# Optimization experiments

Hardware: AMD Instinct MI355X
Metric: run time of the kernel (lower is better)

## Reference

```python
import jax, jax.numpy as jnp
import numpy as np

B, S, D = 8, 4096, 256


def setup_inputs() -> dict:
    key = jax.random.key(0)
    kq, kk, kv, kb = jax.random.split(key, 4)
    q = jax.random.normal(kq, (B, S, D), dtype=jnp.float32)
    k = jax.random.normal(kk, (B, S, D), dtype=jnp.float32)
    v = jax.random.normal(kv, (B, S, D), dtype=jnp.float32)
    beta = jax.random.uniform(kb, (B, S), dtype=jnp.float32)
    return {"q": q, "k": k, "v": v, "beta": beta}


def reference(q, k, v, beta):
    # Delta-rule linear attention recurrence:
    #   h_t = beta_t * h_{t-1} + k_t^T v_t   (h: [B, D, D])
    #   o_t = q_t @ h_t                      (o: [B, D])
    dtype = q.dtype
    b, s, d = q.shape
    h0 = jnp.zeros((b, d, d), dtype=dtype)

    def step(h, inp):
        q_t, k_t, v_t, b_t = inp  # q_t/k_t/v_t: [B, D], b_t: [B]
        h = h * b_t[:, None, None] + jnp.einsum('bi,bj->bij', k_t, v_t)
        o_t = jnp.einsum('bi,bij->bj', q_t, h)
        return h, o_t

    xs = (q.transpose(1, 0, 2), k.transpose(1, 0, 2),
          v.transpose(1, 0, 2), beta.T)  # time-major
    _, out = jax.lax.scan(step, h0, xs)  # out: [S, B, D]
    return out.transpose(1, 0, 2)  # [B, S, D]
```

## Files before the change

### kernel.cpp

```cpp
#include <hip/hip_runtime.h>
#include <hip/hip_bf16.h>
#include <math.h>


#define B_ 8
#define S_ 4096
#define D_ 256
#define L_ 128
#define C_ (S_ / L_)
#define BC_ (B_ * C_)
#define STK 66

typedef __attribute__((ext_vector_type(8))) short s8v;
typedef __attribute__((ext_vector_type(4))) float f4v;
typedef unsigned short u16;
typedef unsigned int u32;

__device__ __forceinline__ u32 pk2(float lo, float hi) {
  union { __hip_bfloat162 h; u32 u; } cv;
  cv.h = __float22bfloat162_rn(make_float2(lo, hi));
  return cv.u;
}
__device__ __forceinline__ s8v pack8(const float4 a, const float4 b) {
  union { u32 u[4]; s8v v; } r;
  r.u[0] = pk2(a.x, a.y); r.u[1] = pk2(a.z, a.w);
  r.u[2] = pk2(b.x, b.y); r.u[3] = pk2(b.z, b.w);
  return r.v;
}

__global__ __launch_bounds__(512, 4) void ks_summary8(
    const float* __restrict__ kg, const float* __restrict__ vg,
    const float* __restrict__ beta, u16* __restrict__ A,
    float* __restrict__ P)
{
  __shared__ float ls[L_];
  __shared__ __align__(16) u16 U[2][256 * STK];

  const int bc = blockIdx.x;
  const int b = bc / C_, c = bc % C_;
  const int tid = threadIdx.x;
  const float* betap = beta + (size_t)b * S_ + (size_t)c * L_;
  const float* kbase = kg + ((size_t)b * S_ + (size_t)c * L_) * D_;
  const float* vbase = vg + ((size_t)b * S_ + (size_t)c * L_) * D_;

  const int hh = tid >> 8;
  const int t2 = tid & 255;
  const int iLs = t2 & 7;
  const int s0s = (t2 >> 3) * 2;
  const int sg = hh * 64 + s0s;

  float bx0 = 1.f, bx1 = 1.f;
  if (tid < 64) { bx0 = betap[tid]; bx1 = betap[64 + tid]; }

  float4 kp[16];
  {
    const float* k0 = kbase + (size_t)sg * D_;
#pragma unroll
    for (int p = 0; p < 8; ++p) {
      const int i0 = p * 32 + iLs * 4;
      kp[2 * p]     = *(const float4*)(k0 + i0);
      kp[2 * p + 1] = *(const float4*)(k0 + D_ + i0);
    }
  }

  if (tid < 64) {
    float x = log2f(fmaxf(bx0, 1e-30f));
#pragma unroll
    for (int off = 1; off < 64; off <<= 1) {
      float y = __shfl_up(x, off);
      if (tid >= off) x += y;
    }
    ls[tid] = x;
    const float tot0 = __shfl(x, 63);
    float z = log2f(fmaxf(bx1, 1e-30f));
#pragma unroll
    for (int off = 1; off < 64; off <<= 1) {
      float y = __shfl_up(z, off);
      if (tid >= off) z += y;
    }
    ls[64 + tid] = z + tot0;
  }
  __syncthreads();
  const float ltot = ls[L_ - 1];
  if (tid == 0) P[bc] = exp2f(ltot);

  {
    const float w0 = exp2f(ltot - ls[sg]);
    const float w1 = exp2f(ltot - ls[sg + 1]);
    u16* dst = U[hh];
#pragma unroll
    for (int p = 0; p < 8; ++p) {
      const int i0 = p * 32 + iLs * 4;
      const float4 a0 = kp[2 * p], a1 = kp[2 * p + 1];
      *(u32*)&dst[(i0 + 0) * STK + s0s] = pk2(a0.x * w0, a1.x * w1);
      *(u32*)&dst[(i0 + 1) * STK + s0s] = pk2(a0.y * w0, a1.y * w1);
      *(u32*)&dst[(i0 + 2) * STK + s0s] = pk2(a0.z * w0, a1.z * w1);
      *(u32*)&dst[(i0 + 3) * STK + s0s] = pk2(a0.w * w0, a1.w * w1);
    }
  }
  __syncthreads();

  const int lane = tid & 63, wave = tid >> 6;
  const int quad = lane >> 4, l15 = lane & 15;
  const int i0w = wave * 32;

  float4 vb[8];
  {
    const float* v0 = vbase + (size_t)sg * D_;
#pragma unroll
    for (int p = 0; p < 4; ++p) {
      const int i0 = p * 32 + iLs * 4;
      vb[2 * p]     = *(const float4*)(v0 + i0);
      vb[2 * p + 1] = *(const float4*)(v0 + D_ + i0);
    }
  }

  s8v af[2][4];
#pragma unroll
  for (int mt = 0; mt < 2; ++mt)
#pragma unroll
    for (int ks = 0; ks < 4; ++ks)
      af[mt][ks] = *(const s8v*)&U[ks >> 1][(i0w + mt * 16 + l15) * STK +
                                            (ks & 1) * 32 + quad * 8];
  __syncthreads();

  {
    u16* dst = U[hh];
#pragma unroll
    for (int p = 0; p < 4; ++p) {
      const int i0 = p * 32 + iLs * 4;
      const float4 a0 = vb[2 * p], a1 = vb[2 * p + 1];
      *(u32*)&dst[(i0 + 0) * STK + s0s] = pk2(a0.x, a1.x);
      *(u32*)&dst[(i0 + 1) * STK + s0s] = pk2(a0.y, a1.y);
      *(u32*)&dst[(i0 + 2) * STK + s0s] = pk2(a0.z, a1.z);
      *(u32*)&dst[(i0 + 3) * STK + s0s] = pk2(a0.w, a1.w);
    }
    const float* v0 = vbase + (size_t)sg * D_;
#pragma unroll
    for (int p = 4; p < 8; ++p) {
      const int i0 = p * 32 + iLs * 4;
      const float4 a0 = *(const float4*)(v0 + i0);
      const float4 a1 = *(const float4*)(v0 + D_ + i0);
      *(u32*)&dst[(i0 + 0) * STK + s0s] = pk2(a0.x, a1.x);
      *(u32*)&dst[(i0 + 1) * STK + s0s] = pk2(a0.y, a1.y);
      *(u32*)&dst[(i0 + 2) * STK + s0s] = pk2(a0.z, a1.z);
      *(u32*)&dst[(i0 + 3) * STK + s0s] = pk2(a0.w, a1.w);
    }
  }
  __syncthreads();

  u16* Ab = A + (size_t)bc * D_ * D_;

  for (int ng = 0; ng < 4; ++ng) {
    f4v acc[2][4];
#pragma unroll
    for (int mt = 0; mt < 2; ++mt)
#pragma unroll
      for (int nt = 0; nt < 4; ++nt) acc[mt][nt] = (f4v){0.f, 0.f, 0.f, 0.f};

#pragma unroll
    for (int ks = 0; ks < 4; ++ks) {
      const int so = (ks & 1) * 32 + quad * 8;
      s8v bv[4];
#pragma unroll
      for (int nt = 0; nt < 4; ++nt)
        bv[nt] = *(const s8v*)&U[ks >> 1][(ng * 64 + nt * 16 + l15) * STK + so];
#pragma unroll
      for (int mt = 0; mt < 2; ++mt)
#pragma unroll
        for (int nt = 0; nt < 4; ++nt)
          acc[mt][nt] = __builtin_amdgcn_mfma_f32_16x16x32_bf16(
              af[mt][ks], bv[nt], acc[mt][nt], 0, 0, 0);
    }
#pragma unroll
    for (int mt = 0; mt < 2; ++mt)
#pragma unroll
      for (int nt = 0; nt < 4; ++nt) {
        const int jl = ng * 64 + nt * 16 + l15;
        uint2 w;
        w.x = pk2(acc[mt][nt][0], acc[mt][nt][1]);
        w.y = pk2(acc[mt][nt][2], acc[mt][nt][3]);
        *(uint2*)&Ab[(size_t)jl * D_ + i0w + mt * 16 + quad * 4] = w;
      }
  }
}

__global__ __launch_bounds__(256) void ks_scan8(
    u16* __restrict__ A, const float* __restrict__ P)
{
  const int g = blockIdx.x;
  const int b = g >> 6;
  const int unit = ((g & 63) << 8) + threadIdx.x;
  u16* base = A + (size_t)b * ((size_t)C_ * D_ * D_) + (size_t)unit * 4;
  const float* Pb = P + b * C_;

  uint2 d[C_];
#pragma unroll
  for (int c = 0; c < C_; ++c)
    d[c] = *(const uint2*)(base + (size_t)c * (D_ * D_));

  float h0 = 0.f, h1 = 0.f, h2 = 0.f, h3 = 0.f;
#pragma unroll
  for (int c = 0; c < C_; ++c) {
    const float pc = Pb[c];
    const uint2 u = d[c];
    const float a0 = __uint_as_float(u.x << 16);
    const float a1 = __uint_as_float(u.x & 0xFFFF0000u);
    const float a2 = __uint_as_float(u.y << 16);
    const float a3 = __uint_as_float(u.y & 0xFFFF0000u);
    d[c].x = pk2(h0, h1);
    d[c].y = pk2(h2, h3);
    h0 = fmaf(pc, h0, a0); h1 = fmaf(pc, h1, a1);
    h2 = fmaf(pc, h2, a2); h3 = fmaf(pc, h3, a3);
  }
#pragma unroll
  for (int c = 0; c < C_; ++c)
    *(uint2*)(base + (size_t)c * (D_ * D_)) = d[c];
}

__global__ __launch_bounds__(512, 2) void ks_output8(
    const float* __restrict__ qg, const float* __restrict__ kg,
    const float* __restrict__ vg, const float* __restrict__ beta,
    const u16* __restrict__ Hg, float* __restrict__ outg)
{
  __shared__ float ls[L_];
  __shared__ float cv[L_];
  __shared__ __align__(16) u16 QB[L_ * 264];
  __shared__ __align__(16) u16 Tm[L_ * 136];
  __shared__ __align__(16) u16 VT[256 * STK];

  const int bc = blockIdx.x;
  const int b = bc / C_, c = bc % C_;
  const int tid = threadIdx.x;
  const float* betap = beta + (size_t)b * S_ + (size_t)c * L_;
  const float* qbase = qg + ((size_t)b * S_ + (size_t)c * L_) * D_;
  const float* kbase = kg + ((size_t)b * S_ + (size_t)c * L_) * D_;
  const float* vbase = vg + ((size_t)b * S_ + (size_t)c * L_) * D_;
  const u16* Hb = Hg + (size_t)bc * D_ * D_;

  float bx0 = 1.f, bx1 = 1.f;
  if (tid < 64) { bx0 = betap[tid]; bx1 = betap[64 + tid]; }

  const int qt = tid >> 2, qc = (tid & 3) * 8;
  float4 qp[16];
  {
    const float* src = qbase + (size_t)qt * D_ + qc;
#pragma unroll
    for (int p = 0; p < 8; ++p) {
      qp[2 * p]     = *(const float4*)(src + p * 32);
      qp[2 * p + 1] = *(const float4*)(src + p * 32 + 4);
    }
  }
  const int iL3 = tid & 15;
  const int s03 = ((tid >> 4) & 31) * 2;
  float4 vp0[8];
  {
    const float* a0 = vbase + (size_t)s03 * D_;
#pragma unroll
    for (int p = 0; p < 4; ++p) {
      const int i0 = p * 64 + iL3 * 4;
      vp0[2 * p]     = *(const float4*)(a0 + i0);
      vp0[2 * p + 1] = *(const float4*)(a0 + D_ + i0);
    }
  }

  if (tid < 64) {
    float x = log2f(fmaxf(bx0, 1e-30f));
#pragma unroll
    for (int off = 1; off < 64; off <<= 1) {
      float y = __shfl_up(x, off);
      if (tid >= off) x += y;
    }
    ls[tid] = x;
    const float tot0 = __shfl(x, 63);
    float z = log2f(fmaxf(bx1, 1e-30f));
#pragma unroll
    for (int off = 1; off < 64; off <<= 1) {
      float y = __shfl_up(z, off);
      if (tid >= off) z += y;
    }
    ls[64 + tid] = z + tot0;
  }

#pragma unroll
  for (int p = 0; p < 8; ++p)
    *(s8v*)&QB[qt * 264 + qc + p * 32] = pack8(qp[2 * p], qp[2 * p + 1]);
  __syncthreads();
  if (tid < L_) cv[tid] = exp2f(ls[tid]);

  const int lane = tid & 63, wave = tid >> 6;
  const int quad = lane >> 4, l15 = lane & 15;
  const int j0w = wave * 32;

  {
    const int mA = wave * 16;
    f4v accA[8];
#pragma unroll
    for (int i = 0; i < 8; ++i) accA[i] = (f4v){0.f, 0.f, 0.f, 0.f};
#pragma unroll
    for (int kd = 0; kd < 8; ++kd) {
      const int d0 = kd * 32 + quad * 8;
      const float* krow = kbase + (size_t)(mA + l15) * D_ + d0;
      const s8v afr = pack8(*(const float4*)krow, *(const float4*)(krow + 4));
#pragma unroll
      for (int nt = 0; nt < 8; ++nt) {
        const s8v bf = *(const s8v*)&QB[(nt * 16 + l15) * 264 + d0];
        accA[nt] = __builtin_amdgcn_mfma_f32_16x16x32_bf16(afr, bf, accA[nt],
                                                           0, 0, 0);
      }
    }
#pragma unroll
    for (int nt = 0; nt < 8; ++nt) {
      const int t = nt * 16 + l15;
      const float lt = ls[t];
      const int s0 = mA + quad * 4;
      float v4[4];
#pragma unroll
      for (int r = 0; r < 4; ++r) {
        const int s = s0 + r;
        v4[r] = (s <= t) ? accA[nt][r] * exp2f(lt - ls[s]) : 0.f;
      }
      uint2 w;
      w.x = pk2(v4[0], v4[1]);
      w.y = pk2(v4[2], v4[3]);
      *(uint2*)&Tm[t * 136 + s0] = w;
    }
  }

  {
#pragma unroll
    for (int p = 0; p < 4; ++p) {
      const int i0 = p * 64 + iL3 * 4;
      const float4 a0 = vp0[2 * p], a1 = vp0[2 * p + 1];
      *(u32*)&VT[(i0 + 0) * STK + s03] = pk2(a0.x, a1.x);
      *(u32*)&VT[(i0 + 1) * STK + s03] = pk2(a0.y, a1.y);
      *(u32*)&VT[(i0 + 2) * STK + s03] = pk2(a0.z, a1.z);
      *(u32*)&VT[(i0 + 3) * STK + s03] = pk2(a0.w, a1.w);
    }
  }

  s8v hc[2];
#pragma unroll
  for (int mt = 0; mt < 2; ++mt)
    hc[mt] = *(const s8v*)(Hb + (size_t)(j0w + mt * 16 + l15) * D_ + quad * 8);

  __syncthreads();

  float4 vp1[8];
  {
    const float* b0 = vbase + (size_t)(64 + s03) * D_;
#pragma unroll
    for (int p = 0; p < 4; ++p) {
      const int i0 = p * 64 + iL3 * 4;
      vp1[2 * p]     = *(const float4*)(b0 + i0);
      vp1[2 * p + 1] = *(const float4*)(b0 + D_ + i0);
    }
  }

  f4v acc[2][8];
#pragma unroll
  for (int mt = 0; mt < 2; ++mt)
#pragma unroll
    for (int nt = 0; nt < 8; ++nt) acc[mt][nt] = (f4v){0.f, 0.f, 0.f, 0.f};

#pragma unroll
  for (int ks = 0; ks < 8; ++ks) {
    const int io = ks * 32 + quad * 8;
    s8v hn[2] = {hc[0], hc[1]};
    if (ks < 7) {
#pragma unroll
      for (int mt = 0; mt < 2; ++mt)
        hn[mt] = *(const s8v*)(Hb + (size_t)(j0w + mt * 16 + l15) * D_ +
                               io + 32);
    }
    s8v bfq[8];
#pragma unroll
    for (int nt = 0; nt < 8; ++nt)
      bfq[nt] = *(const s8v*)&QB[(nt * 16 + l15) * 264 + io];
#pragma unroll
    for (int mt = 0; mt < 2; ++mt)
#pragma unroll
      for (int nt = 0; nt < 8; ++nt)
        acc[mt][nt] = __builtin_amdgcn_mfma_f32_16x16x32_bf16(
            hc[mt], bfq[nt], acc[mt][nt], 0, 0, 0);
    hc[0] = hn[0]; hc[1] = hn[1];
  }
#pragma unroll
  for (int nt = 0; nt < 8; ++nt) {
    const float ct = cv[nt * 16 + l15];
#pragma unroll
    for (int mt = 0; mt < 2; ++mt) {
      acc[mt][nt][0] *= ct; acc[mt][nt][1] *= ct;
      acc[mt][nt][2] *= ct; acc[mt][nt][3] *= ct;
    }
  }

#pragma unroll
  for (int ks = 0; ks < 2; ++ks) {
    const int so = ks * 32 + quad * 8;
    s8v afv[2], bfv[8];
#pragma unroll
    for (int mt = 0; mt < 2; ++mt)
      afv[mt] = *(const s8v*)&VT[(j0w + mt * 16 + l15) * STK + so];
#pragma unroll
    for (int nt = 0; nt < 8; ++nt)
      bfv[nt] = *(const s8v*)&Tm[(nt * 16 + l15) * 136 + so];
#pragma unroll
    for (int mt = 0; mt < 2; ++mt)
#pragma unroll
      for (int nt = 0; nt < 8; ++nt)
        acc[mt][nt] = __builtin_amdgcn_mfma_f32_16x16x32_bf16(
            afv[mt], bfv[nt], acc[mt][nt], 0, 0, 0);
  }

  __syncthreads();
  {
#pragma unroll
    for (int p = 0; p < 4; ++p) {
      const int i0 = p * 64 + iL3 * 4;
      const float4 a0 = vp1[2 * p], a1 = vp1[2 * p + 1];
      *(u32*)&VT[(i0 + 0) * STK + s03] = pk2(a0.x, a1.x);
      *(u32*)&VT[(i0 + 1) * STK + s03] = pk2(a0.y, a1.y);
      *(u32*)&VT[(i0 + 2) * STK + s03] = pk2(a0.z, a1.z);
      *(u32*)&VT[(i0 + 3) * STK + s03] = pk2(a0.w, a1.w);
    }
  }
  __syncthreads();
#pragma unroll
  for (int ks = 0; ks < 2; ++ks) {
    const int so = ks * 32 + quad * 8;
    s8v afv[2], bfv[8];
#pragma unroll
    for (int mt = 0; mt < 2; ++mt)
      afv[mt] = *(const s8v*)&VT[(j0w + mt * 16 + l15) * STK + so];
#pragma unroll
    for (int nt = 0; nt < 8; ++nt)
      bfv[nt] = *(const s8v*)&Tm[(nt * 16 + l15) * 136 + 64 + so];
#pragma unroll
    for (int mt = 0; mt < 2; ++mt)
#pragma unroll
      for (int nt = 0; nt < 8; ++nt)
        acc[mt][nt] = __builtin_amdgcn_mfma_f32_16x16x32_bf16(
            afv[mt], bfv[nt], acc[mt][nt], 0, 0, 0);
  }

  float* ob = outg + ((size_t)b * S_ + (size_t)c * L_) * D_;
#pragma unroll
  for (int mt = 0; mt < 2; ++mt)
#pragma unroll
    for (int nt = 0; nt < 8; ++nt) {
      const int t = nt * 16 + l15;
      const int j0 = j0w + mt * 16 + quad * 4;
      float4 o;
      o.x = acc[mt][nt][0]; o.y = acc[mt][nt][1];
      o.z = acc[mt][nt][2]; o.w = acc[mt][nt][3];
      *(float4*)(ob + (size_t)t * D_ + j0) = o;
    }
}

extern "C" void kernel_launch(void* const* d_in, const int* in_sizes, int n_in,
                              void* d_out, int out_size, void* d_ws,
                              size_t ws_size, hipStream_t stream) {
  const float* q = (const float*)d_in[0];
  const float* k = (const float*)d_in[1];
  const float* v = (const float*)d_in[2];
  const float* beta = (const float*)d_in[3];
  float* out = (float*)d_out;

  u16* A = (u16*)d_ws;
  float* P = (float*)((char*)d_ws + (size_t)BC_ * D_ * D_ * sizeof(u16));

  ks_summary8<<<dim3(BC_), dim3(512), 0, stream>>>(k, v, beta, A, P);
  ks_scan8<<<dim3(512), dim3(256), 0, stream>>>(A, P);
  ks_output8<<<dim3(BC_), dim3(512), 0, stream>>>(q, k, v, beta, A, out);
}
```

Before: 173.7 us.

## Alias output-kernel shared buffers and defer V transpose to raise occupancy

The output kernel now overlays the Q tile, the V-transpose tile and the intra-chunk score tile in one shared array, cutting LDS per block roughly in half. The intra-chunk scores stay packed in registers until after the H·Q product, and the V load and transpose are moved after that GEMM. The launch bound is raised to 4 blocks per CU, and the cumulative-decay exponentials are computed inside the prefix-scan wave. The grid has only 256 blocks, so the added occupancy may go unused. The tighter register budget, with a 64-register accumulator plus the held score registers, risks spilling.

```diff
diff --git a/kernel.cpp b/kernel.cpp
--- a/kernel.cpp
+++ b/kernel.cpp
@@ -28,7 +28,7 @@
   return r.v;
 }
 
-__global__ __launch_bounds__(512, 4) void ks_summary8(
+__global__ __launch_bounds__(512, 4) void ks_summary9(
     const float* __restrict__ kg, const float* __restrict__ vg,
     const float* __restrict__ beta, u16* __restrict__ A,
     float* __restrict__ P)
@@ -185,7 +185,7 @@
   }
 }
 
-__global__ __launch_bounds__(256) void ks_scan8(
+__global__ __launch_bounds__(256) void ks_scan9(
     u16* __restrict__ A, const float* __restrict__ P)
 {
   const int g = blockIdx.x;
@@ -218,16 +218,14 @@
     *(uint2*)(base + (size_t)c * (D_ * D_)) = d[c];
 }
 
-__global__ __launch_bounds__(512, 2) void ks_output8(
+__global__ __launch_bounds__(512, 4) void ks_output9(
     const float* __restrict__ qg, const float* __restrict__ kg,
     const float* __restrict__ vg, const float* __restrict__ beta,
     const u16* __restrict__ Hg, float* __restrict__ outg)
 {
   __shared__ float ls[L_];
   __shared__ float cv[L_];
-  __shared__ __align__(16) u16 QB[L_ * 264];
-  __shared__ __align__(16) u16 Tm[L_ * 136];
-  __shared__ __align__(16) u16 VT[256 * STK];
+  __shared__ __align__(16) u16 raw[34304];
 
   const int bc = blockIdx.x;
   const int b = bc / C_, c = bc % C_;
@@ -251,18 +249,6 @@
       qp[2 * p + 1] = *(const float4*)(src + p * 32 + 4);
     }
   }
-  const int iL3 = tid & 15;
-  const int s03 = ((tid >> 4) & 31) * 2;
-  float4 vp0[8];
-  {
-    const float* a0 = vbase + (size_t)s03 * D_;
-#pragma unroll
-    for (int p = 0; p < 4; ++p) {
-      const int i0 = p * 64 + iL3 * 4;
-      vp0[2 * p]     = *(const float4*)(a0 + i0);
-      vp0[2 * p + 1] = *(const float4*)(a0 + D_ + i0);
-    }
-  }
 
   if (tid < 64) {
     float x = log2f(fmaxf(bx0, 1e-30f));
@@ -272,6 +258,7 @@
       if (tid >= off) x += y;
     }
     ls[tid] = x;
+    cv[tid] = exp2f(x);
     const float tot0 = __shfl(x, 63);
     float z = log2f(fmaxf(bx1, 1e-30f));
 #pragma unroll
@@ -280,20 +267,22 @@
       if (tid >= off) z += y;
     }
     ls[64 + tid] = z + tot0;
-  }
-
+    cv[64 + tid] = exp2f(z + tot0);
+  }
+
+  u16* QB = raw;
 #pragma unroll
   for (int p = 0; p < 8; ++p)
     *(s8v*)&QB[qt * 264 + qc + p * 32] = pack8(qp[2 * p], qp[2 * p + 1]);
   __syncthreads();
-  if (tid < L_) cv[tid] = exp2f(ls[tid]);
 
   const int lane = tid & 63, wave = tid >> 6;
   const int quad = lane >> 4, l15 = lane & 15;
   const int j0w = wave * 32;
-
-  {
-    const int mA = wave * 16;
+  const int mA = wave * 16;
+
+  uint2 tpk[8];
+  {
     f4v accA[8];
 #pragma unroll
     for (int i = 0; i < 8; ++i) accA[i] = (f4v){0.f, 0.f, 0.f, 0.f};
@@ -320,22 +309,8 @@
         const int s = s0 + r;
         v4[r] = (s <= t) ? accA[nt][r] * exp2f(lt - ls[s]) : 0.f;
       }
-      uint2 w;
-      w.x = pk2(v4[0], v4[1]);
-      w.y = pk2(v4[2], v4[3]);
-      *(uint2*)&Tm[t * 136 + s0] = w;
-    }
-  }
-
-  {
-#pragma unroll
-    for (int p = 0; p < 4; ++p) {
-      const int i0 = p * 64 + iL3 * 4;
-      const float4 a0 = vp0[2 * p], a1 = vp0[2 * p + 1];
-      *(u32*)&VT[(i0 + 0) * STK + s03] = pk2(a0.x, a1.x);
-      *(u32*)&VT[(i0 + 1) * STK + s03] = pk2(a0.y, a1.y);
-      *(u32*)&VT[(i0 + 2) * STK + s03] = pk2(a0.z, a1.z);
-      *(u32*)&VT[(i0 + 3) * STK + s03] = pk2(a0.w, a1.w);
+      tpk[nt].x = pk2(v4[0], v4[1]);
+      tpk[nt].y = pk2(v4[2], v4[3]);
     }
   }
 
@@ -343,19 +318,6 @@
 #pragma unroll
   for (int mt = 0; mt < 2; ++mt)
     hc[mt] = *(const s8v*)(Hb + (size_t)(j0w + mt * 16 + l15) * D_ + quad * 8);
-
-  __syncthreads();
-
-  float4 vp1[8];
-  {
-    const float* b0 = vbase + (size_t)(64 + s03) * D_;
-#pragma unroll
-    for (int p = 0; p < 4; ++p) {
-      const int i0 = p * 64 + iL3 * 4;
-      vp1[2 * p]     = *(const float4*)(b0 + i0);
-      vp1[2 * p + 1] = *(const float4*)(b0 + D_ + i0);
-    }
-  }
 
   f4v acc[2][8];
 #pragma unroll
@@ -394,6 +356,47 @@
       acc[mt][nt][2] *= ct; acc[mt][nt][3] *= ct;
     }
   }
+
+  __syncthreads();
+
+  u16* VT = raw;
+  u16* Tm = raw + 16896;
+  const int iL3 = tid & 15;
+  const int s03 = ((tid >> 4) & 31) * 2;
+
+  {
+    const float* a0 = vbase + (size_t)s03 * D_;
+    float4 f0[4], f1[4];
+#pragma unroll
+    for (int p = 0; p < 4; ++p) {
+      const int i0 = p * 64 + iL3 * 4;
+      f0[p] = *(const float4*)(a0 + i0);
+      f1[p] = *(const float4*)(a0 + D_ + i0);
+    }
+#pragma unroll
+    for (int nt = 0; nt < 8; ++nt)
+      *(uint2*)&Tm[(nt * 16 + l15) * 136 + mA + quad * 4] = tpk[nt];
+#pragma unroll
+    for (int p = 0; p < 4; ++p) {
+      const int i0 = p * 64 + iL3 * 4;
+      *(u32*)&VT[(i0 + 0) * STK + s03] = pk2(f0[p].x, f1[p].x);
+      *(u32*)&VT[(i0 + 1) * STK + s03] = pk2(f0[p].y, f1[p].y);
+      *(u32*)&VT[(i0 + 2) * STK + s03] = pk2(f0[p].z, f1[p].z);
+      *(u32*)&VT[(i0 + 3) * STK + s03] = pk2(f0[p].w, f1[p].w);
+    }
+  }
+
+  float4 vp1[8];
+  {
+    const float* b0 = vbase + (size_t)(64 + s03) * D_;
+#pragma unroll
+    for (int p = 0; p < 4; ++p) {
+      const int i0 = p * 64 + iL3 * 4;
+      vp1[2 * p]     = *(const float4*)(b0 + i0);
+      vp1[2 * p + 1] = *(const float4*)(b0 + D_ + i0);
+    }
+  }
+  __syncthreads();
 
 #pragma unroll
   for (int ks = 0; ks < 2; ++ks) {
@@ -470,7 +473,7 @@
   u16* A = (u16*)d_ws;
   float* P = (float*)((char*)d_ws + (size_t)BC_ * D_ * D_ * sizeof(u16));
 
-  ks_summary8<<<dim3(BC_), dim3(512), 0, stream>>>(k, v, beta, A, P);
-  ks_scan8<<<dim3(512), dim3(256), 0, stream>>>(A, P);
-  ks_output8<<<dim3(BC_), dim3(512), 0, stream>>>(q, k, v, beta, A, out);
-}
+  ks_summary9<<<dim3(BC_), dim3(512), 0, stream>>>(k, v, beta, A, P);
+  ks_scan9<<<dim3(512), dim3(256), 0, stream>>>(A, P);
+  ks_output9<<<dim3(BC_), dim3(512), 0, stream>>>(q, k, v, beta, A, out);
+}
```

Measured after the change: 212.4 us. 1.22x slower.
